# Kernel optimization log

Measured on AMD Instinct MI355X. Metric: run time of the kernel, lower is better.

Reference implementation:

```python
import jax, jax.numpy as jnp
import numpy as np

ATT_DIM = 768
N_HEADS = 4
N_LABELS = 2000
NEG_INF = -1e6


def setup_inputs() -> dict:
    key = jax.random.key(0)
    k1, k2, k3, k4, k5, k6 = jax.random.split(key, 6)
    B, S, D = 4, 3072, ATT_DIM
    h = jax.random.normal(k1, (B, S, D), dtype=jnp.float32)
    attention_mask = jnp.ones((B, S), dtype=jnp.int32)
    label_feat = jax.random.normal(k2, (N_LABELS * N_HEADS, D), dtype=jnp.float32)
    # nn.Linear W: weight [D, D], bias [D]
    W_w = jax.random.normal(k3, (D, D), dtype=jnp.float32) * 0.02
    W_b = jnp.zeros((D,), dtype=jnp.float32)
    # classifier: weight [num_labels, D], bias [num_labels]
    cls_w = jax.random.normal(k4, (N_LABELS, D), dtype=jnp.float32) * 0.02
    cls_b = jnp.zeros((N_LABELS,), dtype=jnp.float32)
    return {"h": h, "attention_mask": attention_mask, "label_feat": label_feat,
            "W_w": W_w, "W_b": W_b, "cls_w": cls_w, "cls_b": cls_b}


def reference(h, attention_mask, label_feat, W_w, W_b, cls_w, cls_b):
    # h: [B,S,D]; label_feat: [E*H, D]
    B, S, D = h.shape
    E = label_feat.shape[0] // N_HEADS
    z = jnp.tanh(h @ W_w.T + W_b)                       # [B,S,D]
    u = label_feat.reshape(E, N_HEADS, D)               # [E,H,D]
    # score 'abd,ecd->aebc' -> [B,E,S,H]
    score = jnp.einsum('bsd,ehd->besh', z, u)
    mask = attention_mask.astype(bool)[:, None, :, None]  # [B,1,S,1]
    score = jnp.where(mask, score, NEG_INF)
    alpha = jax.nn.softmax(score, axis=2)               # softmax over seq
    # m 'abd,aebc->aedc' -> [B,E,D,H]
    m = jnp.einsum('bsd,besh->bedh', h, alpha)
    m = m.max(axis=-1)                                  # head max-pool -> [B,E,D]
    logits = jnp.sum(cls_w[None] * m, axis=2) + cls_b   # [B,E]
    return logits, m
```

## Files before the change

### kernel.cpp

```cpp
#include <hip/hip_runtime.h>
#include <hip/hip_bf16.h>

typedef _Float16 f16;
typedef _Float16 half8 __attribute__((ext_vector_type(8)));
typedef _Float16 half4v __attribute__((ext_vector_type(4)));
typedef float f32x4 __attribute__((ext_vector_type(4)));
typedef float f32x16 __attribute__((ext_vector_type(16)));

#define B_ 4
#define S_ 3072
#define D_ 768
#define E_ 2000
#define NEG_INF -1.0e6f

#define GLD16(gsrc, ldst)                                                     \
  __builtin_amdgcn_global_load_lds(                                           \
      (const __attribute__((address_space(1))) void*)(gsrc),                  \
      (__attribute__((address_space(3))) void*)(ldst), 16, 0, 0)

__global__ __launch_bounds__(256) void k_transpose(const float* __restrict__ h,
                                                   f16* __restrict__ ht) {
  __shared__ f16 tile[64][65];
  int b = blockIdx.z, s0 = blockIdx.x * 64, d0 = blockIdx.y * 64;
  int t = threadIdx.x, tx = t & 63, ty = t >> 6;
  const float* src = h + ((size_t)b * S_ + s0) * D_ + d0;
#pragma unroll
  for (int i = 0; i < 16; ++i) {
    int sl = i * 4 + ty;
    tile[sl][tx] = (f16)src[(size_t)sl * D_ + tx];
  }
  __syncthreads();
  f16* dst = ht + ((size_t)b * D_ + d0) * S_ + s0;
#pragma unroll
  for (int i = 0; i < 16; ++i) {
    int dl = i * 4 + ty;
    dst[(size_t)dl * S_ + tx] = tile[tx][dl];
  }
}

__global__ __launch_bounds__(256) void k_zgemm(const float* __restrict__ h,
                                               const float* __restrict__ W,
                                               const float* __restrict__ bias,
                                               f16* __restrict__ zb) {
  __shared__ f16 As[64][40];
  __shared__ f16 Bs[64][40];
  int i0 = blockIdx.x * 64, j0 = blockIdx.y * 64;
  int t = threadIdx.x, w = t >> 6, lane = t & 63, g = lane >> 4, li = lane & 15;
  int wi = w >> 1, wj = w & 1;

  f32x4 acc[2][2];
#pragma unroll
  for (int a = 0; a < 2; ++a)
#pragma unroll
    for (int b2 = 0; b2 < 2; ++b2) acc[a][b2] = (f32x4){0.f, 0.f, 0.f, 0.f};

  int srow = t >> 2, scol = (t & 3) * 8;
  const float* pA = h + (size_t)(i0 + srow) * D_ + scol;
  const float* pB = W + (size_t)(j0 + srow) * D_ + scol;

  for (int kc = 0; kc < D_; kc += 32) {
    float4 a0 = *(const float4*)(pA + kc);
    float4 a1 = *(const float4*)(pA + kc + 4);
    float4 b0 = *(const float4*)(pB + kc);
    float4 b1 = *(const float4*)(pB + kc + 4);
    half8 av = {(f16)a0.x, (f16)a0.y, (f16)a0.z, (f16)a0.w,
                (f16)a1.x, (f16)a1.y, (f16)a1.z, (f16)a1.w};
    half8 bv = {(f16)b0.x, (f16)b0.y, (f16)b0.z, (f16)b0.w,
                (f16)b1.x, (f16)b1.y, (f16)b1.z, (f16)b1.w};
    *(half8*)&As[srow][scol] = av;
    *(half8*)&Bs[srow][scol] = bv;
    __syncthreads();
#pragma unroll
    for (int it = 0; it < 2; ++it) {
      half8 af = *(const half8*)&As[wi * 32 + it * 16 + li][g * 8];
#pragma unroll
      for (int jt = 0; jt < 2; ++jt) {
        half8 bf = *(const half8*)&Bs[wj * 32 + jt * 16 + li][g * 8];
        acc[it][jt] =
            __builtin_amdgcn_mfma_f32_16x16x32_f16(af, bf, acc[it][jt], 0, 0, 0);
      }
    }
    __syncthreads();
  }
#pragma unroll
  for (int it = 0; it < 2; ++it) {
#pragma unroll
    for (int jt = 0; jt < 2; ++jt) {
      int jj = j0 + wj * 32 + jt * 16 + li;
      float bsv = bias[jj];
#pragma unroll
      for (int r = 0; r < 4; ++r) {
        int ii = i0 + wi * 32 + it * 16 + g * 4 + r;
        float v = acc[it][jt][r] + bsv;
        zb[(size_t)ii * D_ + jj] = (f16)tanhf(v);
      }
    }
  }
}

__global__ __launch_bounds__(512)
void k_attn(const float* __restrict__ lf,
            const f16* __restrict__ zb,
            const f16* __restrict__ ht,
            const int* __restrict__ amask,
            float* __restrict__ out_m) {
  __shared__ __align__(16) char Lds[66304];
  char* KsB = Lds;
  char* CpB = Lds + 49152;
  char* PtB = Lds + 61440;
  float* FacB = (float*)(Lds + 65536);
  float* LfinB = (float*)(Lds + 65792);
  int* MskI = (int*)(Lds + 66048);

  const int fid = blockIdx.x;
  const int x2 = fid & 7, u = fid >> 3;
  const int b = x2 >> 1;
  const int qtile = (x2 & 1) * 64 + u;
  if (qtile >= 125) return;
  const int q0 = qtile * 64;
  const int e0 = qtile * 16;

  const int t = threadIdx.x, w = t >> 6, l = t & 63;
  const int l31 = l & 31, h = l >> 5, h16 = h * 16;
  const int qh = w & 1, kq = w >> 1;
  const int dh = w;

  half8 qf[12];
  {
    const float* qp = lf + (size_t)(q0 + qh * 32 + l31) * D_ + kq * 192 + h * 8;
#pragma unroll
    for (int kf = 0; kf < 12; ++kf) {
      float4 v0 = *(const float4*)(qp + kf * 16);
      float4 v1 = *(const float4*)(qp + kf * 16 + 4);
      qf[kf] = (half8){(f16)v0.x, (f16)v0.y, (f16)v0.z, (f16)v0.w,
                       (f16)v1.x, (f16)v1.y, (f16)v1.z, (f16)v1.w};
    }
  }

  int klds[6], kgsw[6];
#pragma unroll
  for (int k = 0; k < 6; ++k) {
    int lin = (w * 6 + k) * 1024 + l * 16;
    int row = lin / 1536;
    int xo = lin - row * 1536;
    klds[k] = lin;
    kgsw[k] = row * 1536 + (xo ^ ((row & 7) << 4));
  }

  const int am7 = (l & 7) << 4;
  const int abase = l31 * 1536 + kq * 384;

  const int rswz = ((l31 >> 1) & 3) << 4;
  const int cqoff = l31 * 64;
  const int csl = (kq >= 1) ? ((kq - 1) * 2 + qh) : 0;

  const char* zbB = (const char*)zb + (size_t)b * S_ * 1536;
  const f16* vbase = ht + ((size_t)b * D_ + dh * 96 + l31) * S_ + h * 8;

#pragma unroll
  for (int k = 0; k < 6; ++k) GLD16(zbB + kgsw[k], KsB + klds[k]);
  if (t < 32) MskI[t] = amask[b * S_ + t];
  asm volatile("s_waitcnt vmcnt(0)" ::: "memory");
  __syncthreads();

  float mreg = -3.0e38f, lreg = 0.0f;
  f32x16 oacc[2][3];
#pragma unroll
  for (int a = 0; a < 2; ++a)
#pragma unroll
    for (int d = 0; d < 3; ++d)
#pragma unroll
      for (int j = 0; j < 16; ++j) oacc[a][d][j] = 0.f;

  half8 Vb[6];

  for (int i = 0; i < 96; ++i) {
    const int s0 = i * 32;
    const int s0n = (i < 95) ? s0 + 32 : 0;

    int mnext = (t < 32) ? amask[b * S_ + s0n + t] : 0;

    if (i > 0) {
      f32x4 frv[2][4];
#pragma unroll
      for (int q2 = 0; q2 < 2; ++q2)
#pragma unroll
        for (int rr = 0; rr < 4; ++rr)
          frv[q2][rr] = *(const f32x4*)(FacB + q2 * 32 + rr * 8 + h * 4);
#pragma unroll
      for (int q2 = 0; q2 < 2; ++q2)
#pragma unroll
        for (int dt = 0; dt < 3; ++dt)
#pragma unroll
          for (int j = 0; j < 16; ++j)
            oacc[q2][dt][j] *= frv[q2][j >> 2][j & 3];
      half8 pa[2][2];
#pragma unroll
      for (int q2 = 0; q2 < 2; ++q2)
#pragma unroll
        for (int ss = 0; ss < 2; ++ss)
          pa[q2][ss] = *(const half8*)(PtB + q2 * 2048 + cqoff +
                                       ((ss * 32 + h16) ^ rswz));
      __builtin_amdgcn_s_setprio(1);
#pragma unroll
      for (int dt = 0; dt < 3; ++dt)
#pragma unroll
        for (int ss = 0; ss < 2; ++ss)
#pragma unroll
          for (int q2 = 0; q2 < 2; ++q2)
            oacc[q2][dt] = __builtin_amdgcn_mfma_f32_32x32x16_f16(
                pa[q2][ss], Vb[dt * 2 + ss], oacc[q2][dt], 0, 0, 0);
      __builtin_amdgcn_s_setprio(0);
    }

    {
      const f16* vp = vbase + s0;
#pragma unroll
      for (int dt = 0; dt < 3; ++dt)
#pragma unroll
        for (int ss = 0; ss < 2; ++ss)
          Vb[dt * 2 + ss] = *(const half8*)(vp + (size_t)dt * 32 * S_ + ss * 16);
    }

    f32x16 ca;
#pragma unroll
    for (int j = 0; j < 16; ++j) ca[j] = 0.f;
    __builtin_amdgcn_s_setprio(1);
#pragma unroll
    for (int kf = 0; kf < 12; ++kf) {
      half8 a = *(const half8*)(KsB + abase + ((kf * 32 + h16) ^ am7));
      ca = __builtin_amdgcn_mfma_f32_32x32x16_f16(a, qf[kf], ca, 0, 0, 0);
    }
    __builtin_amdgcn_s_setprio(0);

    if (kq != 0) {
      char* cp = CpB + csl * 2048 + cqoff;
#pragma unroll
      for (int rr = 0; rr < 4; ++rr) {
        half4v pk = {(f16)ca[4 * rr], (f16)ca[4 * rr + 1], (f16)ca[4 * rr + 2],
                     (f16)ca[4 * rr + 3]};
        *(half4v*)(cp + ((rr * 16 + h * 8) ^ rswz)) = pk;
      }
    }
    asm volatile("s_waitcnt lgkmcnt(0)" ::: "memory");
    __builtin_amdgcn_s_barrier();

    {
      const char* src = zbB + (size_t)s0n * 1536;
#pragma unroll
      for (int k = 0; k < 6; ++k) GLD16(src + kgsw[k], KsB + klds[k]);
    }
    if (kq == 0) {
#pragma unroll
      for (int kk = 1; kk < 4; ++kk) {
        const char* sp = CpB + ((kk - 1) * 2 + qh) * 2048 + cqoff;
#pragma unroll
        for (int rr = 0; rr < 4; ++rr) {
          half4v pk = *(const half4v*)(sp + ((rr * 16 + h * 8) ^ rswz));
          ca[4 * rr + 0] += (float)pk[0];
          ca[4 * rr + 1] += (float)pk[1];
          ca[4 * rr + 2] += (float)pk[2];
          ca[4 * rr + 3] += (float)pk[3];
        }
      }
      const int* mk = MskI + (i & 1) * 32;
      float vmax = -3.0e38f;
#pragma unroll
      for (int rr = 0; rr < 4; ++rr) {
        int4 m4 = *(const int4*)(mk + rr * 8 + h * 4);
#pragma unroll
        for (int j = 0; j < 4; ++j) {
          float sv = ca[4 * rr + j];
          if (!((&m4.x)[j])) sv = NEG_INF;
          ca[4 * rr + j] = sv;
          vmax = fmaxf(vmax, sv);
        }
      }
      vmax = fmaxf(vmax, __shfl_xor(vmax, 32));
      float Mn = fmaxf(mreg, vmax);
      float fec = __expf(mreg - Mn);
      mreg = Mn;
      float ts = 0.f;
#pragma unroll
      for (int j = 0; j < 16; ++j) {
        ca[j] = __expf(ca[j] - Mn);
        ts += ca[j];
      }
      ts += __shfl_xor(ts, 32);
      lreg = lreg * fec + ts;
      if (l < 32) FacB[qh * 32 + l] = fec;
      char* pw = PtB + qh * 2048 + cqoff;
#pragma unroll
      for (int rr = 0; rr < 4; ++rr) {
        half4v pk = {(f16)ca[4 * rr], (f16)ca[4 * rr + 1], (f16)ca[4 * rr + 2],
                     (f16)ca[4 * rr + 3]};
        *(half4v*)(pw + ((rr * 16 + h * 8) ^ rswz)) = pk;
      }
    }
    if (t < 32) MskI[((i + 1) & 1) * 32 + t] = mnext;
    asm volatile("s_waitcnt vmcnt(0) lgkmcnt(0)" ::: "memory");
    __builtin_amdgcn_s_barrier();
  }

  {
    f32x4 frv[2][4];
#pragma unroll
    for (int q2 = 0; q2 < 2; ++q2)
#pragma unroll
      for (int rr = 0; rr < 4; ++rr)
        frv[q2][rr] = *(const f32x4*)(FacB + q2 * 32 + rr * 8 + h * 4);
#pragma unroll
    for (int q2 = 0; q2 < 2; ++q2)
#pragma unroll
      for (int dt = 0; dt < 3; ++dt)
#pragma unroll
        for (int j = 0; j < 16; ++j)
          oacc[q2][dt][j] *= frv[q2][j >> 2][j & 3];
    half8 pa[2][2];
#pragma unroll
    for (int q2 = 0; q2 < 2; ++q2)
#pragma unroll
      for (int ss = 0; ss < 2; ++ss)
        pa[q2][ss] = *(const half8*)(PtB + q2 * 2048 + cqoff +
                                     ((ss * 32 + h16) ^ rswz));
#pragma unroll
    for (int dt = 0; dt < 3; ++dt)
#pragma unroll
      for (int ss = 0; ss < 2; ++ss)
#pragma unroll
        for (int q2 = 0; q2 < 2; ++q2)
          oacc[q2][dt] = __builtin_amdgcn_mfma_f32_32x32x16_f16(
              pa[q2][ss], Vb[dt * 2 + ss], oacc[q2][dt], 0, 0, 0);
  }

  if (kq == 0 && l < 32) LfinB[qh * 32 + l] = lreg;
  __syncthreads();

  f32x4 rlv[2][4];
#pragma unroll
  for (int q2 = 0; q2 < 2; ++q2)
#pragma unroll
    for (int rr = 0; rr < 4; ++rr) {
      f32x4 lv = *(const f32x4*)(LfinB + q2 * 32 + rr * 8 + h * 4);
      rlv[q2][rr] =
          (f32x4){1.0f / lv[0], 1.0f / lv[1], 1.0f / lv[2], 1.0f / lv[3]};
    }
#pragma unroll
  for (int q2 = 0; q2 < 2; ++q2)
#pragma unroll
    for (int dt = 0; dt < 3; ++dt)
#pragma unroll
      for (int rr = 0; rr < 4; ++rr) {
        float mv = oacc[q2][dt][4 * rr + 0] * rlv[q2][rr][0];
        mv = fmaxf(mv, oacc[q2][dt][4 * rr + 1] * rlv[q2][rr][1]);
        mv = fmaxf(mv, oacc[q2][dt][4 * rr + 2] * rlv[q2][rr][2]);
        mv = fmaxf(mv, oacc[q2][dt][4 * rr + 3] * rlv[q2][rr][3]);
        int e_loc = q2 * 8 + rr * 2 + h;
        out_m[((size_t)b * E_ + e0 + e_loc) * D_ + dh * 96 + dt * 32 + l31] = mv;
      }
}

__global__ __launch_bounds__(256) void k_logits(const float* __restrict__ cw,
                                                const float* __restrict__ cb,
                                                const float* __restrict__ m,
                                                float* __restrict__ out) {
  int t = threadIdx.x, w = t >> 6, lane = t & 63;
  int rid = blockIdx.x * 4 + w;
  int b = rid / E_, e = rid - b * E_;
  const float* mr = m + (size_t)rid * D_;
  const float* cr = cw + (size_t)e * D_;
  float acc = 0.f;
#pragma unroll
  for (int i = 0; i < 12; ++i) acc += cr[i * 64 + lane] * mr[i * 64 + lane];
#pragma unroll
  for (int off = 32; off >= 1; off >>= 1) acc += __shfl_xor(acc, off);
  if (lane == 0) out[rid] = acc + cb[e];
}

extern "C" void kernel_launch(void* const* d_in, const int* in_sizes, int n_in,
                              void* d_out, int out_size, void* d_ws, size_t ws_size,
                              hipStream_t stream) {
  const float* h = (const float*)d_in[0];
  const int* amask = (const int*)d_in[1];
  const float* lf = (const float*)d_in[2];
  const float* Ww = (const float*)d_in[3];
  const float* Wb = (const float*)d_in[4];
  const float* cw = (const float*)d_in[5];
  const float* cb = (const float*)d_in[6];
  float* out = (float*)d_out;

  f16* zb = (f16*)d_ws;
  f16* ht = (f16*)((char*)d_ws + 18874368);

  k_transpose<<<dim3(48, 12, 4), 256, 0, stream>>>(h, ht);
  k_zgemm<<<dim3(192, 12), 256, 0, stream>>>(h, Ww, Wb, zb);
  k_attn<<<512, 512, 0, stream>>>(lf, zb, ht, amask, out + 8000);
  k_logits<<<2000, 256, 0, stream>>>(cw, cb, out + 8000, out);
}
```

Measured before the change: 614.9 us.

## Double-buffer K tile in LDS and spread softmax across all waves

The K (z) tile buffer in LDS is doubled so the next tile's global-to-LDS loads are issued before the current score MFMAs rather than after the barrier. This lets the loads overlap compute. The online softmax is also redistributed: every wave writes its partial scores, and all 8 waves each reduce a slice of rows with 8-lane shuffles, replacing the version where only the kq==0 waves did reduction and exp. This roughly doubles LDS use to about 117 KB per block, which may limit occupancy, and adds one more partial-score slot per wave.

```diff
diff --git a/kernel.cpp b/kernel.cpp
--- a/kernel.cpp
+++ b/kernel.cpp
@@ -104,13 +104,13 @@
             const f16* __restrict__ ht,
             const int* __restrict__ amask,
             float* __restrict__ out_m) {
-  __shared__ __align__(16) char Lds[66304];
+  __shared__ __align__(16) char Lds[119552];
   char* KsB = Lds;
-  char* CpB = Lds + 49152;
-  char* PtB = Lds + 61440;
-  float* FacB = (float*)(Lds + 65536);
-  float* LfinB = (float*)(Lds + 65792);
-  int* MskI = (int*)(Lds + 66048);
+  char* CpB = Lds + 98304;
+  char* PtB = Lds + 114688;
+  float* FacB = (float*)(Lds + 118784);
+  float* LfinB = (float*)(Lds + 119040);
+  int* MskI = (int*)(Lds + 119296);
 
   const int fid = blockIdx.x;
   const int x2 = fid & 7, u = fid >> 3;
@@ -152,7 +152,12 @@
 
   const int rswz = ((l31 >> 1) & 3) << 4;
   const int cqoff = l31 * 64;
-  const int csl = (kq >= 1) ? ((kq - 1) * 2 + qh) : 0;
+
+  const int qh_s = w >> 2, qoct = w & 3;
+  const int qrow = qoct * 8 + (l >> 3);
+  const int swzr = ((qrow >> 1) & 3) << 4;
+  const int roff = qrow * 64 + ((8 * (l & 7)) ^ swzr);
+  const int qabs = qh_s * 32 + qrow;
 
   const char* zbB = (const char*)zb + (size_t)b * S_ * 1536;
   const f16* vbase = ht + ((size_t)b * D_ + dh * 96 + l31) * S_ + h * 8;
@@ -177,6 +182,8 @@
   for (int i = 0; i < 96; ++i) {
     const int s0 = i * 32;
     const int s0n = (i < 95) ? s0 + 32 : 0;
+    const char* ksC = KsB + (i & 1) * 49152;
+    char* ksN = KsB + ((i & 1) ^ 1) * 49152;
 
     int mnext = (t < 32) ? amask[b * S_ + s0n + t] : 0;
 
@@ -222,19 +229,26 @@
           Vb[dt * 2 + ss] = *(const half8*)(vp + (size_t)dt * 32 * S_ + ss * 16);
     }
 
+    {
+      const char* src = zbB + (size_t)s0n * 1536;
+#pragma unroll
+      for (int k = 0; k < 6; ++k) GLD16(src + kgsw[k], ksN + klds[k]);
+    }
+    __builtin_amdgcn_sched_barrier(0);
+
     f32x16 ca;
 #pragma unroll
     for (int j = 0; j < 16; ++j) ca[j] = 0.f;
     __builtin_amdgcn_s_setprio(1);
 #pragma unroll
     for (int kf = 0; kf < 12; ++kf) {
-      half8 a = *(const half8*)(KsB + abase + ((kf * 32 + h16) ^ am7));
+      half8 a = *(const half8*)(ksC + abase + ((kf * 32 + h16) ^ am7));
       ca = __builtin_amdgcn_mfma_f32_32x32x16_f16(a, qf[kf], ca, 0, 0, 0);
     }
     __builtin_amdgcn_s_setprio(0);
 
-    if (kq != 0) {
-      char* cp = CpB + csl * 2048 + cqoff;
+    {
+      char* cp = CpB + w * 2048 + cqoff;
 #pragma unroll
       for (int rr = 0; rr < 4; ++rr) {
         half4v pk = {(f16)ca[4 * rr], (f16)ca[4 * rr + 1], (f16)ca[4 * rr + 2],
@@ -246,56 +260,39 @@
     __builtin_amdgcn_s_barrier();
 
     {
-      const char* src = zbB + (size_t)s0n * 1536;
-#pragma unroll
-      for (int k = 0; k < 6; ++k) GLD16(src + kgsw[k], KsB + klds[k]);
-    }
-    if (kq == 0) {
-#pragma unroll
-      for (int kk = 1; kk < 4; ++kk) {
-        const char* sp = CpB + ((kk - 1) * 2 + qh) * 2048 + cqoff;
-#pragma unroll
-        for (int rr = 0; rr < 4; ++rr) {
-          half4v pk = *(const half4v*)(sp + ((rr * 16 + h * 8) ^ rswz));
-          ca[4 * rr + 0] += (float)pk[0];
-          ca[4 * rr + 1] += (float)pk[1];
-          ca[4 * rr + 2] += (float)pk[2];
-          ca[4 * rr + 3] += (float)pk[3];
-        }
-      }
-      const int* mk = MskI + (i & 1) * 32;
-      float vmax = -3.0e38f;
-#pragma unroll
-      for (int rr = 0; rr < 4; ++rr) {
-        int4 m4 = *(const int4*)(mk + rr * 8 + h * 4);
-#pragma unroll
-        for (int j = 0; j < 4; ++j) {
-          float sv = ca[4 * rr + j];
-          if (!((&m4.x)[j])) sv = NEG_INF;
-          ca[4 * rr + j] = sv;
-          vmax = fmaxf(vmax, sv);
-        }
-      }
-      vmax = fmaxf(vmax, __shfl_xor(vmax, 32));
-      float Mn = fmaxf(mreg, vmax);
+      float p0 = 0.f, p1 = 0.f, p2 = 0.f, p3 = 0.f;
+#pragma unroll
+      for (int kk = 0; kk < 4; ++kk) {
+        half4v pk = *(const half4v*)(CpB + (kk * 2 + qh_s) * 2048 + roff);
+        p0 += (float)pk[0];
+        p1 += (float)pk[1];
+        p2 += (float)pk[2];
+        p3 += (float)pk[3];
+      }
+      int4 m4 = *(const int4*)(MskI + (i & 1) * 32 + 4 * (l & 7));
+      if (!m4.x) p0 = NEG_INF;
+      if (!m4.y) p1 = NEG_INF;
+      if (!m4.z) p2 = NEG_INF;
+      if (!m4.w) p3 = NEG_INF;
+      float pmax = fmaxf(fmaxf(p0, p1), fmaxf(p2, p3));
+      pmax = fmaxf(pmax, __shfl_xor(pmax, 1));
+      pmax = fmaxf(pmax, __shfl_xor(pmax, 2));
+      pmax = fmaxf(pmax, __shfl_xor(pmax, 4));
+      float Mn = fmaxf(mreg, pmax);
       float fec = __expf(mreg - Mn);
       mreg = Mn;
-      float ts = 0.f;
-#pragma unroll
-      for (int j = 0; j < 16; ++j) {
-        ca[j] = __expf(ca[j] - Mn);
-        ts += ca[j];
-      }
-      ts += __shfl_xor(ts, 32);
+      p0 = __expf(p0 - Mn);
+      p1 = __expf(p1 - Mn);
+      p2 = __expf(p2 - Mn);
+      p3 = __expf(p3 - Mn);
+      float ts = p0 + p1 + p2 + p3;
+      ts += __shfl_xor(ts, 1);
+      ts += __shfl_xor(ts, 2);
+      ts += __shfl_xor(ts, 4);
       lreg = lreg * fec + ts;
-      if (l < 32) FacB[qh * 32 + l] = fec;
-      char* pw = PtB + qh * 2048 + cqoff;
-#pragma unroll
-      for (int rr = 0; rr < 4; ++rr) {
-        half4v pk = {(f16)ca[4 * rr], (f16)ca[4 * rr + 1], (f16)ca[4 * rr + 2],
-                     (f16)ca[4 * rr + 3]};
-        *(half4v*)(pw + ((rr * 16 + h * 8) ^ rswz)) = pk;
-      }
+      if ((l & 7) == 0) FacB[qabs] = fec;
+      *(half4v*)(PtB + qh_s * 2048 + roff) =
+          (half4v){(f16)p0, (f16)p1, (f16)p2, (f16)p3};
     }
     if (t < 32) MskI[((i + 1) & 1) * 32 + t] = mnext;
     asm volatile("s_waitcnt vmcnt(0) lgkmcnt(0)" ::: "memory");
@@ -333,7 +330,7 @@
               pa[q2][ss], Vb[dt * 2 + ss], oacc[q2][dt], 0, 0, 0);
   }
 
-  if (kq == 0 && l < 32) LfinB[qh * 32 + l] = lreg;
+  if ((l & 7) == 0) LfinB[qabs] = lreg;
   __syncthreads();
 
   f32x4 rlv[2][4];
```

New measurement: 660.4 us. 7.4% more time.
